# Kernel tuning notes

Measured on AMD Instinct MI355X. Metric: run time of the kernel, lower is better.

The kernel has to match this reference:

```python
import jax, jax.numpy as jnp
from jax import lax
import numpy as np

B, C_IN, C_OUT, H, W = 16, 64, 64, 160, 160
K, STRIDE, PAD, DIL, SHIFT = 3, 1, 1, 1, 1


def setup_inputs() -> dict:
    key = jax.random.key(0)
    kx, kw = jax.random.split(key)
    x = jax.random.normal(kx, (B, C_IN, H, W), dtype=jnp.float32)
    weight = jax.random.normal(kw, (C_OUT, C_IN, K, K), dtype=jnp.float32)
    return {"x": x, "weight": weight}


def reference(x, weight):
    Bn, C, Hh, Ww = x.shape
    # zero-pad spatially by shift_distance on all sides (matches F.pad)
    xp = jnp.pad(x, ((0, 0), (0, 0), (SHIFT, SHIFT), (SHIFT, SHIFT)))
    Hp, Wp = Hh + 2 * SHIFT, Ww + 2 * SHIFT
    # shifts list: (dx, dy) for channel groups c % 5
    dxs = jnp.array([0, SHIFT, 0, -SHIFT, 0])
    dys = jnp.array([0, 0, SHIFT, 0, -SHIFT])
    cmod = jnp.arange(C) % 5
    dy = dys[cmod]  # [C] roll along H (dim 2)
    dx = dxs[cmod]  # [C] roll along W (dim 3)
    # torch.roll semantics: out[h, w] = in[(h - dy) % Hp, (w - dx) % Wp]
    row = (jnp.arange(Hp)[None, :] - dy[:, None]) % Hp  # [C, Hp]
    col = (jnp.arange(Wp)[None, :] - dx[:, None]) % Wp  # [C, Wp]
    # single fused gather over channel-dependent row/col indices
    x_shifted = xp[:, jnp.arange(C)[:, None, None], row[:, :, None], col[:, None, :]]
    out = lax.conv_general_dilated(
        x_shifted, weight,
        window_strides=(STRIDE, STRIDE),
        padding=((PAD, PAD), (PAD, PAD)),
        rhs_dilation=(DIL, DIL),
        dimension_numbers=("NCHW", "OIHW", "NCHW"),
    )
    # crop the extra border introduced by the pre-pad
    return out[:, :, 1:-1, 1:-1]
```

## Files before the change

kernel.cpp:

```cpp
#include <hip/hip_runtime.h>
#include <hip/hip_bf16.h>

#define BATCH 16
#define CIN 64
#define COUT 64
#define HH 160
#define WW 160
#define HP 162
#define WP 162

typedef __attribute__((ext_vector_type(8))) __bf16 bf16x8;
typedef __attribute__((ext_vector_type(4))) float f32x4;
typedef __attribute__((ext_vector_type(8))) unsigned short ushort8;

typedef __attribute__((address_space(1))) const unsigned int gu32;
typedef __attribute__((address_space(3))) unsigned int lu32;

__global__ __launch_bounds__(256) void prep(const float* __restrict__ x,
                                            const float* __restrict__ w,
                                            unsigned short* __restrict__ xs,
                                            unsigned short* __restrict__ wb) {
  __shared__ float lds[64 * 160];

  if (blockIdx.x >= BATCH * HP) {
    int e = (blockIdx.x - BATCH * HP) * 256 + threadIdx.x;
    if (e < 9 * 64 * 64) {
      int tap = e >> 12;
      int o = (e >> 6) & 63;
      int c = e & 63;
      float v = w[((size_t)(o * 64 + c)) * 9 + tap];
      __hip_bfloat16 h = __float2bfloat16(v);
      wb[e] = *reinterpret_cast<unsigned short*>(&h);
    }
    return;
  }

  int y = blockIdx.x % HP;
  int b = blockIdx.x / HP;
  int tid = threadIdx.x;

#pragma unroll
  for (int it = 0; it < 10; ++it) {
    int idx = it * 256 + tid;
    int c = idx / 40;
    int j = idx - c * 40;
    int cm = c % 5;
    int dx = (cm == 1) ? 1 : ((cm == 3) ? -1 : 0);
    int dy = (cm == 2) ? 1 : ((cm == 4) ? -1 : 0);
    int yy = y - dy;
    f32x4 v = {0.f, 0.f, 0.f, 0.f};
    if (yy >= 1 && yy <= HH)
      v = *reinterpret_cast<const f32x4*>(
          x + (((size_t)(b * CIN + c)) * HH + (size_t)(yy - 1)) * WW + j * 4);
    int rot = (c & 31) + dx;
    if (rot < 0) rot += 160;
    int p0 = 4 * j + rot;
#pragma unroll
    for (int e = 0; e < 4; ++e) {
      int p = p0 + e;
      if (p >= 160) p -= 160;
      lds[c * 160 + p] = v[e];
    }
  }
  __syncthreads();

  int cg = tid & 7;
  int xr = tid >> 3;
  int dxe[8], rote[8], rowb[8];
#pragma unroll
  for (int e = 0; e < 8; ++e) {
    int c = cg * 8 + e;
    int cm = c % 5;
    int dx = (cm == 1) ? 1 : ((cm == 3) ? -1 : 0);
    int rot = (c & 31) + dx;
    if (rot < 0) rot += 160;
    dxe[e] = dx;
    rote[e] = rot;
    rowb[e] = c * 160;
  }
  size_t obase = ((size_t)(b * HP + y) * WP) * CIN + cg * 8;
#pragma unroll
  for (int it = 0; it < 6; ++it) {
    int xi = it * 32 + xr;
    if (xi < WP) {
      ushort8 val;
#pragma unroll
      for (int e = 0; e < 8; ++e) {
        int xx = xi - dxe[e] - 1;
        float v = 0.f;
        if (xx >= 0 && xx < WW) {
          int p = rote[e] + xx;
          if (p >= 160) p -= 160;
          v = lds[rowb[e] + p];
        }
        __hip_bfloat16 h = __float2bfloat16(v);
        val[e] = *reinterpret_cast<unsigned short*>(&h);
      }
      *reinterpret_cast<ushort8*>(xs + obase + (size_t)xi * CIN) = val;
    }
  }
}

__global__ __launch_bounds__(256, 3) void conv_mfma(const unsigned short* __restrict__ xs,
                                                    const unsigned short* __restrict__ wb,
                                                    float* __restrict__ out) {
  __shared__ __align__(16) unsigned short lds_in[340 * 64];

  int tj = blockIdx.x, ti = blockIdx.y, b = blockIdx.z;
  int tid = threadIdx.x;
  int y0 = ti * 8, x0 = tj * 32;

  const size_t xs_b = (size_t)b * HP * WP * CIN;
#pragma unroll
  for (int k = 0; k < 11; ++k) {
    int u = k * 256 + tid;
    if (u < 2720) {
      int p = u >> 3;
      int j = (u & 7) ^ (p & 7);
      int pr = p / 34, pc = p - pr * 34;
      const unsigned short* src =
          xs + xs_b + ((size_t)(y0 + pr) * WP + (size_t)(x0 + pc)) * CIN + j * 8;
      __builtin_amdgcn_global_load_lds((gu32*)src, (lu32*)&lds_in[(u & ~63) * 8],
                                       16, 0, 0);
    }
  }
  __syncthreads();

  int wv = tid >> 6;
  int lane = tid & 63;
  int l15 = lane & 15;
  int q = lane >> 4;
  int pb = 2 * wv * 34 + l15;
  const unsigned short* bbase = wb + l15 * 64 + q * 8;

  f32x4 acc[4][4];
#pragma unroll
  for (int a = 0; a < 4; ++a)
#pragma unroll
    for (int bb2 = 0; bb2 < 4; ++bb2) acc[a][bb2] = (f32x4){0.f, 0.f, 0.f, 0.f};

  bf16x8 Ab[2][4];
  bf16x8 Bb[3][4];

#define LOAD_B(buf, t)                                                        \
  {                                                                           \
    const int ch_ = (t) / 9, tap_ = (t) % 9;                                  \
    _Pragma("unroll") for (int nt = 0; nt < 4; ++nt)                          \
        Bb[buf][nt] = *reinterpret_cast<const bf16x8*>(                       \
            bbase + tap_ * 4096 + nt * 1024 + ch_ * 32);                      \
  }

#define LOAD_A(buf, t)                                                        \
  {                                                                           \
    const int ch_ = (t) / 9, ky_ = ((t) % 9) / 3, kx_ = (t) % 3;              \
    _Pragma("unroll") for (int mt = 0; mt < 4; ++mt) {                        \
      int pix = pb + (((mt >> 1) + ky_) * 34 + kx_ + (mt & 1) * 16);          \
      int chunk = (ch_ * 4 + q) ^ (pix & 7);                                  \
      Ab[buf][mt] =                                                           \
          *reinterpret_cast<const bf16x8*>(&lds_in[pix * 64 + chunk * 8]);    \
    }                                                                         \
  }

  LOAD_B(0, 0);
  LOAD_B(1, 1);
  LOAD_A(0, 0);
#pragma unroll
  for (int t = 0; t < 18; ++t) {
    if (t + 2 < 18) LOAD_B((t + 2) % 3, t + 2);
    if (t + 1 < 18) LOAD_A((t + 1) & 1, t + 1);
#pragma unroll
    for (int mt = 0; mt < 4; ++mt)
#pragma unroll
      for (int nt = 0; nt < 4; ++nt)
        acc[mt][nt] = __builtin_amdgcn_mfma_f32_16x16x32_bf16(
            Ab[t & 1][mt], Bb[t % 3][nt], acc[mt][nt], 0, 0, 0);
  }
#undef LOAD_A
#undef LOAD_B

#pragma unroll
  for (int mt = 0; mt < 4; ++mt) {
    int i = y0 + 2 * wv + (mt >> 1);
    int xo = x0 + (mt & 1) * 16 + q * 4;
#pragma unroll
    for (int nt = 0; nt < 4; ++nt) {
      int o = nt * 16 + l15;
      *reinterpret_cast<f32x4*>(out + ((size_t)(b * COUT + o) * HH + (size_t)i) * WW + xo) =
          acc[mt][nt];
    }
  }
}

extern "C" void kernel_launch(void* const* d_in, const int* in_sizes, int n_in,
                              void* d_out, int out_size, void* d_ws, size_t ws_size,
                              hipStream_t stream) {
  const float* x = (const float*)d_in[0];
  const float* w = (const float*)d_in[1];
  float* out = (float*)d_out;

  unsigned short* xs = (unsigned short*)d_ws;
  unsigned short* wb = (unsigned short*)((char*)d_ws + (size_t)BATCH * HP * WP * CIN * 2);

  hipLaunchKernelGGL(prep, dim3(BATCH * HP + 144), dim3(256), 0, stream, x, w, xs, wb);
  hipLaunchKernelGGL(conv_mfma, dim3(5, 20, BATCH), dim3(256), 0, stream, xs, wb, out);
}
```

Baseline: 276.5 us.

## Make conv kernel persistent with double-buffered LDS tiles and resident weights

The conv kernel becomes persistent: 256 blocks each loop over 6-7 output tiles. The next tile's input is prefetched into a second LDS buffer with async global-to-LDS loads while the current tile is computed. All bf16 weights are staged once into swizzled LDS instead of being re-read from global memory per tile. This is meant to hide input-load latency and cut repeated weight fetches, but occupancy drops to one block per CU and the larger LDS footprint limits concurrency. The stage-to-compute ordering relies on a single barrier per tile.

Result: faster. 226.5 us (-18.1%).

```diff
diff --git a/kernel.cpp b/kernel.cpp
--- a/kernel.cpp
+++ b/kernel.cpp
@@ -8,6 +8,8 @@
 #define WW 160
 #define HP 162
 #define WP 162
+
+#define ABUF 21760
 
 typedef __attribute__((ext_vector_type(8))) __bf16 bf16x8;
 typedef __attribute__((ext_vector_type(4))) float f32x4;
@@ -101,94 +103,132 @@
   }
 }
 
-__global__ __launch_bounds__(256, 3) void conv_mfma(const unsigned short* __restrict__ xs,
+__global__ __launch_bounds__(256, 1) void conv_mfma(const unsigned short* __restrict__ xs,
                                                     const unsigned short* __restrict__ wb,
                                                     float* __restrict__ out) {
-  __shared__ __align__(16) unsigned short lds_in[340 * 64];
-
-  int tj = blockIdx.x, ti = blockIdx.y, b = blockIdx.z;
+  __shared__ __align__(16) unsigned short lds_a[ABUF];
+  __shared__ __align__(16) unsigned short lds_b[ABUF];
+  __shared__ __align__(16) unsigned short lds_w[9 * 64 * 64];
+
   int tid = threadIdx.x;
-  int y0 = ti * 8, x0 = tj * 32;
-
-  const size_t xs_b = (size_t)b * HP * WP * CIN;
-#pragma unroll
-  for (int k = 0; k < 11; ++k) {
-    int u = k * 256 + tid;
-    if (u < 2720) {
-      int p = u >> 3;
-      int j = (u & 7) ^ (p & 7);
-      int pr = p / 34, pc = p - pr * 34;
-      const unsigned short* src =
-          xs + xs_b + ((size_t)(y0 + pr) * WP + (size_t)(x0 + pc)) * CIN + j * 8;
-      __builtin_amdgcn_global_load_lds((gu32*)src, (lu32*)&lds_in[(u & ~63) * 8],
-                                       16, 0, 0);
-    }
-  }
-  __syncthreads();
+  int blk = blockIdx.x;
+  int tile0 = (blk & 7) * 32 + (blk >> 3);
+  int ntiles = (tile0 < 64) ? 7 : 6;
 
   int wv = tid >> 6;
   int lane = tid & 63;
   int l15 = lane & 15;
   int q = lane >> 4;
-  int pb = 2 * wv * 34 + l15;
-  const unsigned short* bbase = wb + l15 * 64 + q * 8;
+
+  int goff[11];
+#pragma unroll
+  for (int r = 0; r < 11; ++r) {
+    int u = r * 256 + tid;
+    int p = u >> 3;
+    int j = (u & 7) ^ (p & 7);
+    int pr = p / 34, pc = p - pr * 34;
+    goff[r] = (pr * WP + pc) * CIN + j * 8;
+  }
+
+  int bw0 = l15 * 64 + ((q ^ (l15 & 7)) * 8);
+  int bw1 = l15 * 64 + (((4 + q) ^ (l15 & 7)) * 8);
+
+#define STAGE_TO(BUFARR, T_)                                                   \
+  {                                                                            \
+    int sb_ = (T_) / 100;                                                      \
+    int srr_ = (T_) - sb_ * 100;                                               \
+    int sti_ = srr_ / 5, stj_ = srr_ - sti_ * 5;                               \
+    const unsigned short* srcb_ = xs +                                         \
+        ((size_t)sb_ * HP + (size_t)(sti_ * 8)) * WP * CIN +                   \
+        (size_t)(stj_ * 32) * CIN;                                             \
+    unsigned short* dst0_ = (BUFARR) + wv * 512;                               \
+    _Pragma("unroll") for (int r = 0; r < 10; ++r)                             \
+        __builtin_amdgcn_global_load_lds((gu32*)(srcb_ + goff[r]),             \
+                                         (lu32*)(dst0_ + r * 2048), 16, 0, 0); \
+    if (tid < 160)                                                             \
+      __builtin_amdgcn_global_load_lds((gu32*)(srcb_ + goff[10]),              \
+                                       (lu32*)(dst0_ + 10 * 2048), 16, 0, 0);  \
+  }
+
+#define LOAD_A(RBUF, bufp, tt)                                                 \
+  {                                                                            \
+    const int ch_ = (tt) / 9, ky_ = ((tt) % 9) / 3, kx_ = (tt) % 3;            \
+    _Pragma("unroll") for (int mt = 0; mt < 4; ++mt) {                         \
+      int pix = 2 * wv * 34 + l15 +                                            \
+                (((mt >> 1) + ky_) * 34 + kx_ + (mt & 1) * 16);                \
+      int chunk = (ch_ * 4 + q) ^ (pix & 7);                                   \
+      Ab[bufp][mt] =                                                           \
+          *reinterpret_cast<const bf16x8*>(&(RBUF)[pix * 64 + chunk * 8]);     \
+    }                                                                          \
+  }
+
+#define LOAD_BW(bufp, tt)                                                      \
+  {                                                                            \
+    const int ch_ = (tt) / 9, tap_ = (tt) % 9;                                 \
+    _Pragma("unroll") for (int nt = 0; nt < 4; ++nt)                           \
+        Bb[bufp][nt] = *reinterpret_cast<const bf16x8*>(                       \
+            &lds_w[tap_ * 4096 + nt * 1024 + (ch_ ? bw1 : bw0)]);              \
+  }
+
+#define TILE_BODY(I_, RBUF, WBUF)                                              \
+  {                                                                            \
+    int t_ = tile0 + 256 * (I_);                                               \
+    int b_ = t_ / 100;                                                         \
+    int rr_ = t_ - b_ * 100;                                                   \
+    int ti_ = rr_ / 5, tj_ = rr_ - ti_ * 5;                                    \
+    int y0_ = ti_ * 8, x0_ = tj_ * 32;                                         \
+    if ((I_) + 1 < ntiles) STAGE_TO(WBUF, tile0 + 256 * ((I_) + 1));           \
+    _Pragma("unroll") for (int a_ = 0; a_ < 4; ++a_)                           \
+      _Pragma("unroll") for (int c2_ = 0; c2_ < 4; ++c2_)                      \
+        acc[a_][c2_] = (f32x4){0.f, 0.f, 0.f, 0.f};                            \
+    LOAD_A(RBUF, 0, 0);                                                        \
+    LOAD_BW(0, 0);                                                             \
+    _Pragma("unroll") for (int tt = 0; tt < 18; ++tt) {                        \
+      if (tt + 1 < 18) {                                                       \
+        LOAD_A(RBUF, (tt + 1) & 1, tt + 1);                                    \
+        LOAD_BW((tt + 1) & 1, tt + 1);                                         \
+      }                                                                        \
+      _Pragma("unroll") for (int mt = 0; mt < 4; ++mt)                         \
+        _Pragma("unroll") for (int nt = 0; nt < 4; ++nt)                       \
+          acc[mt][nt] = __builtin_amdgcn_mfma_f32_16x16x32_bf16(               \
+              Ab[tt & 1][mt], Bb[tt & 1][nt], acc[mt][nt], 0, 0, 0);           \
+    }                                                                          \
+    __syncthreads();                                                           \
+    _Pragma("unroll") for (int mt = 0; mt < 4; ++mt) {                         \
+      int orow_ = y0_ + 2 * wv + (mt >> 1);                                    \
+      int xo_ = x0_ + (mt & 1) * 16 + q * 4;                                   \
+      _Pragma("unroll") for (int nt = 0; nt < 4; ++nt) {                       \
+        int o_ = nt * 16 + l15;                                                \
+        *reinterpret_cast<f32x4*>(                                             \
+            out + ((size_t)(b_ * COUT + o_) * HH + (size_t)orow_) * WW + xo_) = \
+            acc[mt][nt];                                                       \
+      }                                                                        \
+    }                                                                          \
+  }
 
   f32x4 acc[4][4];
-#pragma unroll
-  for (int a = 0; a < 4; ++a)
-#pragma unroll
-    for (int bb2 = 0; bb2 < 4; ++bb2) acc[a][bb2] = (f32x4){0.f, 0.f, 0.f, 0.f};
-
   bf16x8 Ab[2][4];
-  bf16x8 Bb[3][4];
-
-#define LOAD_B(buf, t)                                                        \
-  {                                                                           \
-    const int ch_ = (t) / 9, tap_ = (t) % 9;                                  \
-    _Pragma("unroll") for (int nt = 0; nt < 4; ++nt)                          \
-        Bb[buf][nt] = *reinterpret_cast<const bf16x8*>(                       \
-            bbase + tap_ * 4096 + nt * 1024 + ch_ * 32);                      \
-  }
-
-#define LOAD_A(buf, t)                                                        \
-  {                                                                           \
-    const int ch_ = (t) / 9, ky_ = ((t) % 9) / 3, kx_ = (t) % 3;              \
-    _Pragma("unroll") for (int mt = 0; mt < 4; ++mt) {                        \
-      int pix = pb + (((mt >> 1) + ky_) * 34 + kx_ + (mt & 1) * 16);          \
-      int chunk = (ch_ * 4 + q) ^ (pix & 7);                                  \
-      Ab[buf][mt] =                                                           \
-          *reinterpret_cast<const bf16x8*>(&lds_in[pix * 64 + chunk * 8]);    \
-    }                                                                         \
-  }
-
-  LOAD_B(0, 0);
-  LOAD_B(1, 1);
-  LOAD_A(0, 0);
-#pragma unroll
-  for (int t = 0; t < 18; ++t) {
-    if (t + 2 < 18) LOAD_B((t + 2) % 3, t + 2);
-    if (t + 1 < 18) LOAD_A((t + 1) & 1, t + 1);
-#pragma unroll
-    for (int mt = 0; mt < 4; ++mt)
-#pragma unroll
-      for (int nt = 0; nt < 4; ++nt)
-        acc[mt][nt] = __builtin_amdgcn_mfma_f32_16x16x32_bf16(
-            Ab[t & 1][mt], Bb[t % 3][nt], acc[mt][nt], 0, 0, 0);
-  }
+  bf16x8 Bb[2][4];
+
+  for (int r = 0; r < 18; ++r) {
+    int u = r * 256 + tid;
+    int orow = u >> 3;
+    int jj = (u & 7) ^ (orow & 7);
+    __builtin_amdgcn_global_load_lds((gu32*)(wb + orow * 64 + jj * 8),
+                                     (lu32*)(lds_w + (u & ~63) * 8), 16, 0, 0);
+  }
+  STAGE_TO(lds_a, tile0);
+  __syncthreads();
+
+  for (int i = 0; i < ntiles; i += 2) {
+    TILE_BODY(i, lds_a, lds_b);
+    if (i + 1 < ntiles) TILE_BODY(i + 1, lds_b, lds_a);
+  }
+
+#undef TILE_BODY
+#undef LOAD_BW
 #undef LOAD_A
-#undef LOAD_B
-
-#pragma unroll
-  for (int mt = 0; mt < 4; ++mt) {
-    int i = y0 + 2 * wv + (mt >> 1);
-    int xo = x0 + (mt & 1) * 16 + q * 4;
-#pragma unroll
-    for (int nt = 0; nt < 4; ++nt) {
-      int o = nt * 16 + l15;
-      *reinterpret_cast<f32x4*>(out + ((size_t)(b * COUT + o) * HH + (size_t)i) * WW + xo) =
-          acc[mt][nt];
-    }
-  }
+#undef STAGE_TO
 }
 
 extern "C" void kernel_launch(void* const* d_in, const int* in_sizes, int n_in,
@@ -202,5 +242,5 @@
   unsigned short* wb = (unsigned short*)((char*)d_ws + (size_t)BATCH * HP * WP * CIN * 2);
 
   hipLaunchKernelGGL(prep, dim3(BATCH * HP + 144), dim3(256), 0, stream, x, w, xs, wb);
-  hipLaunchKernelGGL(conv_mfma, dim3(5, 20, BATCH), dim3(256), 0, stream, xs, wb, out);
+  hipLaunchKernelGGL(conv_mfma, dim3(256), dim3(256), 0, stream, xs, wb, out);
 }
```
